# Performance work log

Hardware: AMD Instinct MI355X
Metric: run time of the kernel (lower is better)

The kernel has to match this reference:

```python
import jax, jax.numpy as jnp
import numpy as np

N_EMBD = 1024
N_HEAD = 16

def setup_inputs() -> dict:
    key = jax.random.key(0)
    ks = jax.random.split(key, 5)
    B, T, C = 4, 2048, N_EMBD
    s = 0.02
    return {
        'x': jax.random.normal(ks[0], (B, T, C), jnp.float32),
        'w_attn': jax.random.normal(ks[1], (C, 3 * C), jnp.float32) * s,
        'b_attn': jax.random.normal(ks[2], (3 * C,), jnp.float32) * s,
        'w_proj': jax.random.normal(ks[3], (C, C), jnp.float32) * s,
        'b_proj': jax.random.normal(ks[4], (C,), jnp.float32) * s,
    }

def reference(x, w_attn, b_attn, w_proj, b_proj):
    B, T, C = x.shape
    H = N_HEAD
    D = C // H  # head dim
    qkv = x @ w_attn + b_attn                      # [B,T,3C]
    q, k, v = jnp.split(qkv, 3, axis=-1)
    q = q.reshape(B, T, H, D).transpose(0, 2, 1, 3)  # [B,H,T,D]
    k = k.reshape(B, T, H, D).transpose(0, 2, 1, 3)
    v = v.reshape(B, T, H, D).transpose(0, 2, 1, 3)
    att = jnp.einsum('bhqd,bhkd->bhqk', q, k) * (1.0 / jnp.sqrt(jnp.float32(D)))
    causal = jnp.tril(jnp.ones((T, T), bool))
    att = jnp.where(causal[None, None], att, jnp.float32(-jnp.inf))
    att = jax.nn.softmax(att, axis=-1)
    y = jnp.einsum('bhqk,bhkd->bhqd', att, v)      # [B,H,T,D]
    y = y.transpose(0, 2, 1, 3).reshape(B, T, C)
    return y @ w_proj + b_proj
```

## Files before the change

kernel.cpp:

```cpp
#include <hip/hip_runtime.h>
#include <math.h>

typedef short s16x8 __attribute__((ext_vector_type(8)));
typedef unsigned short u16;
typedef unsigned short u16x4 __attribute__((ext_vector_type(4)));
typedef float f32x4 __attribute__((ext_vector_type(4)));

__device__ __forceinline__ f32x4 mfma16(s16x8 a, s16x8 b, f32x4 c) {
  return __builtin_amdgcn_mfma_f32_16x16x32_bf16(a, b, c, 0, 0, 0);
}

__device__ __forceinline__ u16 f2bf(float f) {
  unsigned u = __builtin_bit_cast(unsigned, f);
  u = (u + 0x7fffu + ((u >> 16) & 1u)) >> 16;
  return (u16)u;
}

__device__ __forceinline__ unsigned pk_trunc(float hi, float lo) {
  return __builtin_amdgcn_perm(__builtin_bit_cast(unsigned, hi),
                               __builtin_bit_cast(unsigned, lo), 0x07060302u);
}

__device__ __forceinline__ void gll16(const void* g, void* l) {
  __builtin_amdgcn_global_load_lds((__attribute__((address_space(1))) void*)(void*)g,
                                   (__attribute__((address_space(3))) void*)l,
                                   16, 0, 0);
}

__device__ __forceinline__ void lds_fence() {
  asm volatile("s_waitcnt lgkmcnt(0)" ::: "memory");
}

__global__ __launch_bounds__(256) void k_convert_x(const float* __restrict__ x,
                                                   u16* __restrict__ xb) {
  int i = (blockIdx.x * 256 + threadIdx.x) * 8;
  const float4* xv = (const float4*)(x + i);
  float4 a = xv[0], b = xv[1];
  union { s16x8 v; u16 s[8]; } r;
  r.s[0] = f2bf(a.x); r.s[1] = f2bf(a.y); r.s[2] = f2bf(a.z); r.s[3] = f2bf(a.w);
  r.s[4] = f2bf(b.x); r.s[5] = f2bf(b.y); r.s[6] = f2bf(b.z); r.s[7] = f2bf(b.w);
  *(s16x8*)(xb + i) = r.v;
}

__global__ __launch_bounds__(256) void k_transpose_w(const float* __restrict__ in,
                                                     u16* __restrict__ out, int R, int C) {
  __shared__ float tile[32][33];
  int c0 = blockIdx.x * 32, r0 = blockIdx.y * 32;
  int tx = threadIdx.x & 31, ty = threadIdx.x >> 5;
#pragma unroll
  for (int s = 0; s < 4; ++s)
    tile[ty + 8 * s][tx] = in[(size_t)(r0 + ty + 8 * s) * C + c0 + tx];
  __syncthreads();
#pragma unroll
  for (int s = 0; s < 4; ++s)
    out[(size_t)(c0 + ty + 8 * s) * R + r0 + tx] = f2bf(tile[tx][ty + 8 * s]);
}

template <int EPI>
__global__ __launch_bounds__(256) void k_gemm(const u16* __restrict__ A,
                                              const u16* __restrict__ Bt,
                                              const float* __restrict__ bias,
                                              float* __restrict__ outp,
                                              u16* __restrict__ q_out,
                                              u16* __restrict__ k_out,
                                              u16* __restrict__ vt_out,
                                              int K, int nIter) {
  __shared__ u16 As[2][4096];
  __shared__ u16 Bs[2][4096];
  int tid = threadIdx.x, w = tid >> 6, l = tid & 63;
  int r = l & 15, qd = l >> 4;
  int id = blockIdx.x;
  int xcd = id & 7, s0 = id >> 3;
  int mBlk = xcd * 8 + (s0 & 7);
  int nBlk = s0 >> 3;
  f32x4 acc[4][4] = {};

  const u16* ga[2]; const u16* gb[2]; int lgrp[2];
#pragma unroll
  for (int qq = 0; qq < 2; ++qq) {
    int grp = 2 * w + qq;
    int rowA = mBlk * 128 + grp * 16 + (l >> 2);
    int rowB = nBlk * 128 + grp * 16 + (l >> 2);
    int kcol = (l & 3) * 8;
    ga[qq] = A + (size_t)rowA * K + kcol;
    gb[qq] = Bt + (size_t)rowB * K + kcol;
    lgrp[qq] = grp * 512;
  }
  int aoff = ((w & 1) * 4) * 512 + r * 32 + qd * 8;
  int boff = ((w >> 1) * 4) * 512 + r * 32 + qd * 8;

  auto stageg = [&](int kt, int buf) {
#pragma unroll
    for (int qq = 0; qq < 2; ++qq) {
      gll16(ga[qq] + kt * 32, As[buf] + lgrp[qq]);
      gll16(gb[qq] + kt * 32, Bs[buf] + lgrp[qq]);
    }
  };

  stageg(0, 0);
  __syncthreads();

  for (int kt = 0; kt < nIter; ++kt) {
    int cur = kt & 1;
    if (kt + 1 < nIter) stageg(kt + 1, cur ^ 1);
    s16x8 af[4], bf[4];
#pragma unroll
    for (int i = 0; i < 4; ++i) af[i] = *(const s16x8*)(As[cur] + aoff + i * 512);
#pragma unroll
    for (int j = 0; j < 4; ++j) bf[j] = *(const s16x8*)(Bs[cur] + boff + j * 512);
#pragma unroll
    for (int i = 0; i < 4; ++i)
#pragma unroll
      for (int j = 0; j < 4; ++j) acc[i][j] = mfma16(af[i], bf[j], acc[i][j]);
    __syncthreads();
  }

  const float QSCALE = 0.125f * 1.44269504088896f;
  int rowBase = mBlk * 128 + (w & 1) * 64;
  int colBase = nBlk * 128 + (w >> 1) * 64;
#pragma unroll
  for (int i = 0; i < 4; ++i) {
#pragma unroll
    for (int j = 0; j < 4; ++j) {
      int col = colBase + j * 16 + r;
      float bv = bias[col];
      float vv[4];
#pragma unroll
      for (int g = 0; g < 4; ++g) vv[g] = acc[i][j][g] + bv;
      int row0 = rowBase + i * 16 + qd * 4;
      if (EPI == 0) {
        int which = col >> 10;
        int rem = col & 1023;
        int hh = rem >> 6, dd = rem & 63;
        int bb = row0 >> 11, tt0 = row0 & 2047;
        if (which == 2) {
          u16x4 pk;
#pragma unroll
          for (int g = 0; g < 4; ++g) pk[g] = f2bf(vv[g]);
          *(u16x4*)(vt_out + (((size_t)(bb * 16 + hh)) * 64 + dd) * 2048 + tt0) = pk;
        } else {
          u16* base = (which == 0) ? q_out : k_out;
#pragma unroll
          for (int g = 0; g < 4; ++g) {
            float v = vv[g];
            if (which == 0) v *= QSCALE;
            base[(((size_t)(bb * 16 + hh)) * 2048 + tt0 + g) * 64 + dd] = f2bf(v);
          }
        }
      } else {
#pragma unroll
        for (int g = 0; g < 4; ++g)
          outp[(size_t)(row0 + g) * 1024 + col] = vv[g];
      }
    }
  }
}

__global__ __launch_bounds__(256, 2) void k_attn(const u16* __restrict__ qg,
                                                 const u16* __restrict__ kg,
                                                 const u16* __restrict__ vtg,
                                                 u16* __restrict__ yg) {
  __shared__ u16 Ks[3][64 * 64];
  __shared__ u16 Vs[3][64 * 64];
  __shared__ u16 Ps[4][64 * 64];

  int bh = blockIdx.y, bb = bh >> 4, hh = bh & 15;
  int bx = blockIdx.x;
  int tid = threadIdx.x, w = tid >> 6, l = tid & 63;
  int r = l & 15, qd = l >> 4;
  int psw = (r & 7) * 8;

  const int chunk[4] = {bx, 15 - bx, 16 + bx, 31 - bx};
  const int nend[4]  = {bx + 1, 16 - bx, 17 + bx, 32 - bx};
  int nmax = 32 - bx;
  int qloc = w * 16 + r;

  s16x8 qf[4][2];
#pragma unroll
  for (int c = 0; c < 4; ++c) {
    int qbase = chunk[c] * 64 + w * 16;
#pragma unroll
    for (int s = 0; s < 2; ++s)
      qf[c][s] = *(const s16x8*)(qg + ((size_t)bh * 2048 + qbase + r) * 64 + s * 32 + qd * 8);
  }

  s16x8 onesf;
#pragma unroll
  for (int e = 0; e < 8; ++e) onesf[e] = (short)0x3F80;

  f32x4 o[4][4] = {};
  f32x4 lacc[4] = {};

  int rl = l >> 3;
  int cg = (l & 7) ^ rl;
  const u16* kbase = kg + (size_t)bh * 2048 * 64;
  const u16* vbase = vtg + (size_t)bh * 64 * 2048;

  auto stage = [&](int kt, int buf) {
    int kk0 = kt * 64;
#pragma unroll
    for (int p = 0; p < 2; ++p) {
      int row = p * 32 + w * 8 + rl;
      gll16(kbase + ((size_t)(kk0 + row)) * 64 + cg * 8, Ks[buf] + p * 2048 + w * 512);
      gll16(vbase + (size_t)row * 2048 + kk0 + cg * 8, Vs[buf] + p * 2048 + w * 512);
    }
  };

  stage(0, 0);
  stage(1, 1);
  asm volatile("s_waitcnt vmcnt(4)" ::: "memory");
  __builtin_amdgcn_s_barrier();

  int cur = 0, b2 = 2;
  for (int kt = 0; kt < nmax; ++kt) {
    int nk = kt + 2;
    nk = (nk < nmax) ? nk : (nmax - 1);
    stage(nk, b2);

    f32x4 sacc[4][4];
#pragma unroll
    for (int c = 0; c < 4; ++c)
      if (kt < nend[c])
#pragma unroll
        for (int j = 0; j < 4; ++j) sacc[c][j] = f32x4{0.f, 0.f, 0.f, 0.f};
    __builtin_amdgcn_s_setprio(1);
#pragma unroll
    for (int s = 0; s < 2; ++s) {
#pragma unroll
      for (int j = 0; j < 4; ++j) {
        s16x8 kf = *(const s16x8*)(Ks[cur] + (16 * j + r) * 64 + ((s * 4 + qd) ^ (r & 7)) * 8);
#pragma unroll
        for (int c = 0; c < 4; ++c)
          if (kt < nend[c]) sacc[c][j] = mfma16(kf, qf[c][s], sacc[c][j]);
      }
    }
    __builtin_amdgcn_s_setprio(0);

#pragma unroll
    for (int c = 0; c < 4; ++c) {
      if (kt >= nend[c]) continue;
      bool needMask = (kt == chunk[c]);
#pragma unroll
      for (int j = 0; j < 4; ++j) {
        float p0, p1, p2, p3;
        if (needMask) {
          int kb0 = 16 * j + 4 * qd;
          p0 = (kb0 + 0 > qloc) ? 0.f : __builtin_amdgcn_exp2f(sacc[c][j][0]);
          p1 = (kb0 + 1 > qloc) ? 0.f : __builtin_amdgcn_exp2f(sacc[c][j][1]);
          p2 = (kb0 + 2 > qloc) ? 0.f : __builtin_amdgcn_exp2f(sacc[c][j][2]);
          p3 = (kb0 + 3 > qloc) ? 0.f : __builtin_amdgcn_exp2f(sacc[c][j][3]);
        } else {
          p0 = __builtin_amdgcn_exp2f(sacc[c][j][0]);
          p1 = __builtin_amdgcn_exp2f(sacc[c][j][1]);
          p2 = __builtin_amdgcn_exp2f(sacc[c][j][2]);
          p3 = __builtin_amdgcn_exp2f(sacc[c][j][3]);
        }
        uint2 pk;
        pk.x = pk_trunc(p1, p0);
        pk.y = pk_trunc(p3, p2);
        *(uint2*)(Ps[w] + (c * 16 + r) * 64 + ((j * 16 + qd * 4) ^ psw)) = pk;
      }
    }
    lds_fence();

    __builtin_amdgcn_s_setprio(1);
#pragma unroll
    for (int s = 0; s < 2; ++s) {
      s16x8 pa[4];
#pragma unroll
      for (int c = 0; c < 4; ++c)
        if (kt < nend[c]) {
          pa[c] = *(const s16x8*)(Ps[w] + (c * 16 + r) * 64 + ((s * 32 + qd * 8) ^ psw));
          lacc[c] = mfma16(onesf, pa[c], lacc[c]);
        }
#pragma unroll
      for (int j = 0; j < 4; ++j) {
        s16x8 vf = *(const s16x8*)(Vs[cur] + (16 * j + r) * 64 + ((s * 4 + qd) ^ (r & 7)) * 8);
#pragma unroll
        for (int c = 0; c < 4; ++c)
          if (kt < nend[c]) o[c][j] = mfma16(vf, pa[c], o[c][j]);
      }
    }
    __builtin_amdgcn_s_setprio(0);

    asm volatile("s_waitcnt vmcnt(4)" ::: "memory");
    __builtin_amdgcn_s_barrier();
    cur = (cur == 2) ? 0 : cur + 1;
    b2 = (b2 == 2) ? 0 : b2 + 1;
  }

#pragma unroll
  for (int c = 0; c < 4; ++c) {
    int qbase = chunk[c] * 64 + w * 16;
    float inv = 1.0f / lacc[c][0];
    size_t rowoff = ((size_t)bb * 2048 + qbase + r) * 1024 + hh * 64;
#pragma unroll
    for (int j = 0; j < 4; ++j) {
      u16x4 yv;
      yv[0] = f2bf(o[c][j][0] * inv);
      yv[1] = f2bf(o[c][j][1] * inv);
      yv[2] = f2bf(o[c][j][2] * inv);
      yv[3] = f2bf(o[c][j][3] * inv);
      *(u16x4*)(yg + rowoff + 16 * j + 4 * qd) = yv;
    }
  }
}

extern "C" void kernel_launch(void* const* d_in, const int* in_sizes, int n_in,
                              void* d_out, int out_size, void* d_ws, size_t ws_size,
                              hipStream_t stream) {
  const float* x      = (const float*)d_in[0];
  const float* w_attn = (const float*)d_in[1];
  const float* b_attn = (const float*)d_in[2];
  const float* w_proj = (const float*)d_in[3];
  const float* b_proj = (const float*)d_in[4];
  float* out = (float*)d_out;

  char* ws = (char*)d_ws;
  size_t off = 0;
  auto alloc = [&](size_t bytes) -> void* {
    void* p = ws + off;
    off += (bytes + 255) & ~(size_t)255;
    return p;
  };
  const size_t BT = 8192, C = 1024;
  u16* xb  = (u16*)alloc(BT * C * 2);
  u16* waT = (u16*)alloc(3072 * 1024 * 2);
  u16* wpT = (u16*)alloc(1024 * 1024 * 2);
  u16* qb  = (u16*)alloc(BT * C * 2);
  u16* kb  = (u16*)alloc(BT * C * 2);
  u16* vtb = (u16*)alloc(BT * C * 2);
  (void)ws_size; (void)in_sizes; (void)n_in; (void)out_size;

  k_convert_x<<<4096, 256, 0, stream>>>(x, xb);
  k_transpose_w<<<dim3(96, 32), 256, 0, stream>>>(w_attn, waT, 1024, 3072);
  k_transpose_w<<<dim3(32, 32), 256, 0, stream>>>(w_proj, wpT, 1024, 1024);
  k_gemm<0><<<1536, 256, 0, stream>>>(xb, waT, b_attn, nullptr, qb, kb, vtb, 1024, 32);
  k_attn<<<dim3(8, 64), 256, 0, stream>>>(qb, kb, vtb, xb );
  k_gemm<1><<<512, 256, 0, stream>>>(xb, wpT, b_proj, out, nullptr, nullptr, nullptr, 1024, 32);
}
```

Baseline: 269.6 us.

## Software-pipeline QK/softmax with PV and remap attention blocks per XCD

```diff
diff --git a/kernel.cpp b/kernel.cpp
--- a/kernel.cpp
+++ b/kernel.cpp
@@ -164,8 +164,12 @@
   __shared__ u16 Vs[3][64 * 64];
   __shared__ u16 Ps[4][64 * 64];
 
-  int bh = blockIdx.y, bb = bh >> 4, hh = bh & 15;
-  int bx = blockIdx.x;
+  int id = blockIdx.x;
+  int xcd = id & 7;
+  int slot = id >> 3;
+  int bx = slot & 7;
+  int bh = ((slot >> 3) << 3) | xcd;
+  int bb = bh >> 4, hh = bh & 15;
   int tid = threadIdx.x, w = tid >> 6, l = tid & 63;
   int r = l & 15, qd = l >> 4;
   int psw = (r & 7) * 8;
@@ -206,17 +210,7 @@
     }
   };
 
-  stage(0, 0);
-  stage(1, 1);
-  asm volatile("s_waitcnt vmcnt(4)" ::: "memory");
-  __builtin_amdgcn_s_barrier();
-
-  int cur = 0, b2 = 2;
-  for (int kt = 0; kt < nmax; ++kt) {
-    int nk = kt + 2;
-    nk = (nk < nmax) ? nk : (nmax - 1);
-    stage(nk, b2);
-
+  auto qk_smax = [&](int kt, int buf) {
     f32x4 sacc[4][4];
 #pragma unroll
     for (int c = 0; c < 4; ++c)
@@ -228,14 +222,13 @@
     for (int s = 0; s < 2; ++s) {
 #pragma unroll
       for (int j = 0; j < 4; ++j) {
-        s16x8 kf = *(const s16x8*)(Ks[cur] + (16 * j + r) * 64 + ((s * 4 + qd) ^ (r & 7)) * 8);
+        s16x8 kf = *(const s16x8*)(Ks[buf] + (16 * j + r) * 64 + ((s * 4 + qd) ^ (r & 7)) * 8);
 #pragma unroll
         for (int c = 0; c < 4; ++c)
           if (kt < nend[c]) sacc[c][j] = mfma16(kf, qf[c][s], sacc[c][j]);
       }
     }
     __builtin_amdgcn_s_setprio(0);
-
 #pragma unroll
     for (int c = 0; c < 4; ++c) {
       if (kt >= nend[c]) continue;
@@ -261,8 +254,9 @@
         *(uint2*)(Ps[w] + (c * 16 + r) * 64 + ((j * 16 + qd * 4) ^ psw)) = pk;
       }
     }
-    lds_fence();
-
+  };
+
+  auto pv = [&](int kt, int buf) {
     __builtin_amdgcn_s_setprio(1);
 #pragma unroll
     for (int s = 0; s < 2; ++s) {
@@ -275,18 +269,28 @@
         }
 #pragma unroll
       for (int j = 0; j < 4; ++j) {
-        s16x8 vf = *(const s16x8*)(Vs[cur] + (16 * j + r) * 64 + ((s * 4 + qd) ^ (r & 7)) * 8);
+        s16x8 vf = *(const s16x8*)(Vs[buf] + (16 * j + r) * 64 + ((s * 4 + qd) ^ (r & 7)) * 8);
 #pragma unroll
         for (int c = 0; c < 4; ++c)
           if (kt < nend[c]) o[c][j] = mfma16(vf, pa[c], o[c][j]);
       }
     }
     __builtin_amdgcn_s_setprio(0);
-
-    asm volatile("s_waitcnt vmcnt(4)" ::: "memory");
-    __builtin_amdgcn_s_barrier();
-    cur = (cur == 2) ? 0 : cur + 1;
-    b2 = (b2 == 2) ? 0 : b2 + 1;
+  };
+
+  stage(0, 0);
+  stage(1, 1);
+  __syncthreads();
+  qk_smax(0, 0);
+  lds_fence();
+
+  int b0 = 0, b1 = 1, b2 = 2;
+  for (int kt = 0; kt < nmax; ++kt) {
+    if (kt + 2 < nmax) stage(kt + 2, b2);
+    pv(kt, b0);
+    if (kt + 1 < nmax) qk_smax(kt + 1, b1);
+    __syncthreads();
+    int t = b0; b0 = b1; b1 = b2; b2 = t;
   }
 
 #pragma unroll
@@ -336,6 +340,6 @@
   k_transpose_w<<<dim3(96, 32), 256, 0, stream>>>(w_attn, waT, 1024, 3072);
   k_transpose_w<<<dim3(32, 32), 256, 0, stream>>>(w_proj, wpT, 1024, 1024);
   k_gemm<0><<<1536, 256, 0, stream>>>(xb, waT, b_attn, nullptr, qb, kb, vtb, 1024, 32);
-  k_attn<<<dim3(8, 64), 256, 0, stream>>>(qb, kb, vtb, xb );
+  k_attn<<<512, 256, 0, stream>>>(qb, kb, vtb, xb );
   k_gemm<1><<<512, 256, 0, stream>>>(xb, wpT, b_proj, out, nullptr, nullptr, nullptr, 1024, 32);
 }
```

New measurement: 264.0 us. -2.1%, faster.
